# Performance work log

Measured on AMD Instinct MI355X. Metric: run time of the kernel, lower is better.

The kernel has to match this reference:

```python
import jax, jax.numpy as jnp
import numpy as np

# dims: batch B, frames F_, spatial tokens N, heads H, head dim D, model dim DIM
B, F_, N, H, D, DIM = 1, 16, 1024, 8, 64, 512


def setup_inputs() -> dict:
    key = jax.random.key(0)
    k1, k2, k3, k4 = jax.random.split(key, 4)
    x = jax.random.normal(k1, (B, F_ * N, DIM), dtype=jnp.float32)
    W_qkv = jax.random.normal(k2, (DIM, 3 * H * D), dtype=jnp.float32) * 0.02
    W_out = jax.random.normal(k3, (H * D, DIM), dtype=jnp.float32) * 0.02
    mask = jax.random.randint(k4, (1, 1, N), 0, 2, dtype=jnp.int32)
    return {"x": x, "W_qkv": W_qkv, "W_out": W_out, "mask": mask, "diag": 1}


def reference(x, W_qkv, W_out, mask, diag):
    scale = D ** -0.5
    qkv = x @ W_qkv                      # [B, F*N, 3*H*D]
    q, k, v = jnp.split(qkv, 3, axis=-1)

    def split_heads(t):                  # 'b n (h d) -> (b h) n d'
        return t.reshape(B, F_ * N, H, D).transpose(0, 2, 1, 3).reshape(B * H, F_ * N, D)

    q, k, v = map(split_heads, (q, k, v))
    q = q * scale

    def axial(t):                        # '(b h) (f n) d -> (b h f) n d'
        return t.reshape(B * H * F_, N, D)

    q, k, v = map(axial, (q, k, v))

    sim = jnp.einsum('bid,bjd->bij', q, k)        # [(B*H*F), N, N]
    neg = -jnp.finfo(sim.dtype).max
    if diag:
        sim = jnp.where(jnp.eye(N, dtype=bool)[None], neg, sim)
    sim = jnp.where(mask == 0, neg, sim)           # padding mask broadcast
    attn = jax.nn.softmax(sim, axis=-1)
    out = jnp.einsum('bij,bjd->bid', attn, v)      # [(B*H*F), N, D]

    # '(b h f) n d -> (b h) (f n) d' then '(b h) n d -> b n (h d)'
    out = out.reshape(B, H, F_ * N, D).transpose(0, 2, 1, 3).reshape(B, F_ * N, H * D)
    return out @ W_out
```

## Files before the change

### kernel.cpp

```cpp
#include <hip/hip_runtime.h>
#include <stdint.h>

typedef __bf16 bf16;
typedef __bf16 bf16x8 __attribute__((ext_vector_type(8)));
typedef float f32x4 __attribute__((ext_vector_type(4)));

__device__ __forceinline__ void gload_lds16(const void* g, void* l) {
    __builtin_amdgcn_global_load_lds((const __attribute__((address_space(1))) void*)g,
                                     (__attribute__((address_space(3))) void*)l, 16, 0, 0);
}

__device__ __forceinline__ float fast_exp2(float x) { return __builtin_amdgcn_exp2f(x); }

__global__ __launch_bounds__(256) void k_cvt(const float* __restrict__ x, bf16* __restrict__ xb, int n8) {
    int i = blockIdx.x * 256 + threadIdx.x;
    if (i >= n8) return;
    const f32x4* p = (const f32x4*)(x + (size_t)i * 8);
    f32x4 a = p[0], b = p[1];
    bf16x8 o;
    o[0] = (bf16)a[0]; o[1] = (bf16)a[1]; o[2] = (bf16)a[2]; o[3] = (bf16)a[3];
    o[4] = (bf16)b[0]; o[5] = (bf16)b[1]; o[6] = (bf16)b[2]; o[7] = (bf16)b[3];
    *(bf16x8*)(xb + (size_t)i * 8) = o;
}

__global__ __launch_bounds__(256) void k_tx(const float* __restrict__ W, bf16* __restrict__ WT, int R, int C) {
    __shared__ float t[32][33];
    int n0 = blockIdx.x * 32, k0 = blockIdx.y * 32;
    int tx = threadIdx.x, ty = threadIdx.y;
    for (int i = 0; i < 32; i += 8) t[ty + i][tx] = W[(size_t)(k0 + ty + i) * C + n0 + tx];
    __syncthreads();
    for (int i = 0; i < 32; i += 8) WT[(size_t)(n0 + ty + i) * R + k0 + tx] = (bf16)t[tx][ty + i];
}

__global__ __launch_bounds__(256) void k_scan(const int* __restrict__ mask, int* __restrict__ idxU,
                                              int* __restrict__ cpos, int* __restrict__ meta) {
    __shared__ int lsum[256];
    int t = threadIdx.x;
    int m[4], s = 0;
#pragma unroll
    for (int e = 0; e < 4; e++) { m[e] = mask[4 * t + e]; s += m[e]; }
    lsum[t] = s;
    __syncthreads();
    for (int off = 1; off < 256; off <<= 1) {
        int v = (t >= off) ? lsum[t - off] : 0;
        __syncthreads();
        lsum[t] += v;
        __syncthreads();
    }
    int run = lsum[t] - s;
#pragma unroll
    for (int e = 0; e < 4; e++) {
        if (m[e]) { idxU[run] = 4 * t + e; cpos[4 * t + e] = run; run++; }
        else cpos[4 * t + e] = -1;
    }
    if (t == 255) { meta[0] = lsum[255]; meta[1] = (lsum[255] + 63) >> 6; }
}

__global__ __launch_bounds__(256) void k_qkv(const bf16* __restrict__ Xb, const bf16* __restrict__ WT,
                                             bf16* __restrict__ Qb, bf16* __restrict__ Kb, bf16* __restrict__ Vb) {
    __shared__ char As[16384], Bs[16384];
    int tid = threadIdx.x, l = tid & 63, w = tid >> 6;
    int wy = w >> 1, wx = w & 1;
    int id = blockIdx.x;
    int wg = (id & 7) * 192 + (id >> 3);
    int bm = (wg / 12) * 128, bn = (wg % 12) * 128;
    int lr = l & 15, kg = l >> 4;
    int p = l & 7, rsub = l >> 3;
    int csrc = p ^ rsub;
    f32x4 acc[4][4] = {};

    for (int k0 = 0; k0 < 512; k0 += 64) {
        __syncthreads();
#pragma unroll
        for (int i = 0; i < 4; i++) {
            int rt = w * 32 + i * 8 + rsub;
            gload_lds16((const char*)Xb + ((size_t)(bm + rt) * 512 + k0) * 2 + csrc * 16,
                        As + w * 4096 + i * 1024 + l * 16);
            gload_lds16((const char*)WT + ((size_t)(bn + rt) * 512 + k0) * 2 + csrc * 16,
                        Bs + w * 4096 + i * 1024 + l * 16);
        }
        __syncthreads();
#pragma unroll
        for (int kk = 0; kk < 2; kk++) {
            bf16x8 af[4], bfr[4];
            int sb = (kk * 4 + kg);
#pragma unroll
            for (int mt = 0; mt < 4; mt++) {
                int r = wy * 64 + mt * 16 + lr;
                af[mt] = *(const bf16x8*)(As + r * 128 + ((sb ^ (lr & 7)) << 4));
            }
#pragma unroll
            for (int nt = 0; nt < 4; nt++) {
                int r = wx * 64 + nt * 16 + lr;
                bfr[nt] = *(const bf16x8*)(Bs + r * 128 + ((sb ^ (lr & 7)) << 4));
            }
#pragma unroll
            for (int mt = 0; mt < 4; mt++)
#pragma unroll
                for (int nt = 0; nt < 4; nt++)
                    acc[mt][nt] = __builtin_amdgcn_mfma_f32_16x16x32_bf16(af[mt], bfr[nt], acc[mt][nt], 0, 0, 0);
        }
    }
#pragma unroll
    for (int mt = 0; mt < 4; mt++) {
#pragma unroll
        for (int nt = 0; nt < 4; nt++) {
            int c = bn + wx * 64 + nt * 16 + lr;
            int which = c >> 9, hd = c & 511, h = hd >> 6, d = hd & 63;
            float qs = (which == 0) ? 0.18033688f : 1.0f;
            bf16* base = (which == 0) ? Qb : (which == 1) ? Kb : Vb;
#pragma unroll
            for (int j = 0; j < 4; j++) {
                int m = bm + wy * 64 + mt * 16 + kg * 4 + j;
                int f = m >> 10, nn = m & 1023;
                base[((size_t)(h * 16 + f) * 1024 + nn) * 64 + d] = (bf16)(acc[mt][nt][j] * qs);
            }
        }
    }
}

__global__ __launch_bounds__(256) void k_gk(const bf16* __restrict__ Kb, bf16* __restrict__ Kc,
                                            const int* __restrict__ idxU, const int* __restrict__ meta) {
    int bp = blockIdx.y;
    int c = blockIdx.x * 32 + (threadIdx.x >> 3);
    int nU = meta[0], nUp = meta[1] << 6;
    if (c >= nUp) return;
    int ch = (threadIdx.x & 7) * 8;
    bf16x8 v = {};
    if (c < nU) {
        int row = idxU[c];
        v = *(const bf16x8*)(Kb + ((size_t)bp * 1024 + row) * 64 + ch);
    }
    *(bf16x8*)(Kc + ((size_t)bp * 1024 + c) * 64 + ch) = v;
}

__global__ __launch_bounds__(256) void k_vtg(const bf16* __restrict__ V, bf16* __restrict__ Vtc,
                                             const int* __restrict__ idxU, const int* __restrict__ meta) {
    __shared__ bf16 t[64][80];
    int bp = blockIdx.y, c0 = blockIdx.x * 64;
    int nU = meta[0], nUp = meta[1] << 6;
    if (c0 >= nUp) return;
    int tid = threadIdx.x;
    int nl = tid >> 2, dc = (tid & 3) * 16;
    int c = c0 + nl;
    bf16x8 a0 = {}, a1 = {};
    if (c < nU) {
        int row = idxU[c];
        const bf16* src = V + ((size_t)bp * 1024 + row) * 64 + dc;
        a0 = *(const bf16x8*)src;
        a1 = *(const bf16x8*)(src + 8);
    }
    *(bf16x8*)&t[nl][dc] = a0;
    *(bf16x8*)&t[nl][dc + 8] = a1;
    __syncthreads();
    int dl = tid >> 2, nc = (tid & 3) * 16;
    bf16x8 o0, o1;
#pragma unroll
    for (int i = 0; i < 8; i++) o0[i] = t[nc + i][dl];
#pragma unroll
    for (int i = 0; i < 8; i++) o1[i] = t[nc + 8 + i][dl];
    bf16* dst = Vtc + ((size_t)bp * 64 + dl) * 1024 + c0 + nc;
    *(bf16x8*)dst = o0;
    *(bf16x8*)(dst + 8) = o1;
}

__global__ __launch_bounds__(512) void k_attn(const bf16* __restrict__ Qb, const bf16* __restrict__ Kc,
                                              const bf16* __restrict__ Vtc, bf16* __restrict__ AO,
                                              const int* __restrict__ cpos, const int* __restrict__ meta,
                                              const int* __restrict__ diagp) {
    __shared__ char Ks[8192], Vs[8192], Ps[16384];
    int tid = threadIdx.x, l = tid & 63, w = tid >> 6;
    int id = blockIdx.x;
    int wg = (id & 7) * 128 + (id >> 3);
    int qt = wg & 7, bp = wg >> 3;
    int lr = l & 15, kg = l >> 4;
    int diag = diagp[0];
    int nU = meta[0], nT = meta[1];

    int nq = qt * 128 + w * 16 + lr;
    const char* Qrow = (const char*)Qb + ((size_t)bp * 1024 + nq) * 128;
    bf16x8 qf0 = *(const bf16x8*)(Qrow + kg * 16);
    bf16x8 qf1 = *(const bf16x8*)(Qrow + 64 + kg * 16);

    int cq[4];
#pragma unroll
    for (int j = 0; j < 4; j++) {
        int qg = qt * 128 + w * 16 + kg * 4 + j;
        cq[j] = diag ? cpos[qg] : -1;
    }

    const char* Kbase = (const char*)Kc + (size_t)bp * 1024 * 128;
    const char* Vbase = (const char*)Vtc + (size_t)bp * 64 * 2048;

    int rs = tid >> 3;
    int cs = (tid & 7) ^ (rs & 7);

    f32x4 o[4] = {};
    f32x4 psum = {0.f, 0.f, 0.f, 0.f};

    for (int kt = 0; kt < nT; kt++) {
        __syncthreads();
        gload_lds16(Kbase + (size_t)(kt * 64 + rs) * 128 + cs * 16, Ks + w * 1024);
        gload_lds16(Vbase + (size_t)rs * 2048 + kt * 128 + cs * 16, Vs + w * 1024);
        __syncthreads();

        f32x4 s[4] = {};
#pragma unroll
        for (int nt = 0; nt < 4; nt++) {
            int r = nt * 16 + lr;
            bf16x8 kf0 = *(const bf16x8*)(Ks + r * 128 + ((kg ^ (r & 7)) << 4));
            bf16x8 kf1 = *(const bf16x8*)(Ks + r * 128 + (((4 + kg) ^ (r & 7)) << 4));
            s[nt] = __builtin_amdgcn_mfma_f32_16x16x32_bf16(qf0, kf0, s[nt], 0, 0, 0);
            s[nt] = __builtin_amdgcn_mfma_f32_16x16x32_bf16(qf1, kf1, s[nt], 0, 0, 0);
        }

        float mf0 = (kt * 64 + lr < nU) ? 1.f : 0.f;
        float mf1 = (kt * 64 + 16 + lr < nU) ? 1.f : 0.f;
        float mf2 = (kt * 64 + 32 + lr < nU) ? 1.f : 0.f;
        float mf3 = (kt * 64 + 48 + lr < nU) ? 1.f : 0.f;
#pragma unroll
        for (int j = 0; j < 4; j++) {
            s[0][j] = fast_exp2(s[0][j]) * mf0;
            s[1][j] = fast_exp2(s[1][j]) * mf1;
            s[2][j] = fast_exp2(s[2][j]) * mf2;
            s[3][j] = fast_exp2(s[3][j]) * mf3;
        }
#pragma unroll
        for (int nt = 0; nt < 4; nt++) {
            int c = kt * 64 + nt * 16 + lr;
#pragma unroll
            for (int j = 0; j < 4; j++)
                if (c == cq[j]) s[nt][j] = 0.f;
        }
#pragma unroll
        for (int j = 0; j < 4; j++) psum[j] += (s[0][j] + s[1][j]) + (s[2][j] + s[3][j]);

#pragma unroll
        for (int nt = 0; nt < 4; nt++)
#pragma unroll
            for (int j = 0; j < 4; j++) {
                int rq = w * 16 + kg * 4 + j;
                int byte = (rq * 128 + (nt * 16 + lr) * 2) ^ ((rq & 7) << 4);
                *(bf16*)(Ps + byte) = (bf16)s[nt][j];
            }

        int rp = w * 16 + lr;
        bf16x8 pf0 = *(const bf16x8*)(Ps + rp * 128 + ((kg ^ (rp & 7)) << 4));
        bf16x8 pf1 = *(const bf16x8*)(Ps + rp * 128 + (((4 + kg) ^ (rp & 7)) << 4));
#pragma unroll
        for (int dt = 0; dt < 4; dt++) {
            int rd = dt * 16 + lr;
            bf16x8 vf0 = *(const bf16x8*)(Vs + rd * 128 + ((kg ^ (rd & 7)) << 4));
            bf16x8 vf1 = *(const bf16x8*)(Vs + rd * 128 + (((4 + kg) ^ (rd & 7)) << 4));
            o[dt] = __builtin_amdgcn_mfma_f32_16x16x32_bf16(pf0, vf0, o[dt], 0, 0, 0);
            o[dt] = __builtin_amdgcn_mfma_f32_16x16x32_bf16(pf1, vf1, o[dt], 0, 0, 0);
        }
    }

#pragma unroll
    for (int off = 1; off < 16; off <<= 1)
#pragma unroll
        for (int j = 0; j < 4; j++) psum[j] += __shfl_xor(psum[j], off, 64);
    float inv[4];
#pragma unroll
    for (int j = 0; j < 4; j++) inv[j] = 1.0f / psum[j];

    int f = bp & 15, h = bp >> 4;
#pragma unroll
    for (int dt = 0; dt < 4; dt++)
#pragma unroll
        for (int j = 0; j < 4; j++) {
            int n = qt * 128 + w * 16 + kg * 4 + j;
            size_t m = (size_t)f * 1024 + n;
            AO[m * 512 + h * 64 + dt * 16 + lr] = (bf16)(o[dt][j] * inv[j]);
        }
}

__global__ __launch_bounds__(256) void k_out(const bf16* __restrict__ Ab, const bf16* __restrict__ WT,
                                             float* __restrict__ out) {
    __shared__ char As[16384], Bs[16384];
    int tid = threadIdx.x, l = tid & 63, w = tid >> 6;
    int wy = w >> 1, wx = w & 1;
    int id = blockIdx.x;
    int wg = (id & 7) * 64 + (id >> 3);
    int bm = (wg / 4) * 128, bn = (wg % 4) * 128;
    int lr = l & 15, kg = l >> 4;
    int p = l & 7, rsub = l >> 3;
    int csrc = p ^ rsub;
    f32x4 acc[4][4] = {};

    for (int k0 = 0; k0 < 512; k0 += 64) {
        __syncthreads();
#pragma unroll
        for (int i = 0; i < 4; i++) {
            int rt = w * 32 + i * 8 + rsub;
            gload_lds16((const char*)Ab + ((size_t)(bm + rt) * 512 + k0) * 2 + csrc * 16,
                        As + w * 4096 + i * 1024 + l * 16);
            gload_lds16((const char*)WT + ((size_t)(bn + rt) * 512 + k0) * 2 + csrc * 16,
                        Bs + w * 4096 + i * 1024 + l * 16);
        }
        __syncthreads();
#pragma unroll
        for (int kk = 0; kk < 2; kk++) {
            bf16x8 af[4], bfr[4];
            int sb = (kk * 4 + kg);
#pragma unroll
            for (int mt = 0; mt < 4; mt++) {
                int r = wy * 64 + mt * 16 + lr;
                af[mt] = *(const bf16x8*)(As + r * 128 + ((sb ^ (lr & 7)) << 4));
            }
#pragma unroll
            for (int nt = 0; nt < 4; nt++) {
                int r = wx * 64 + nt * 16 + lr;
                bfr[nt] = *(const bf16x8*)(Bs + r * 128 + ((sb ^ (lr & 7)) << 4));
            }
#pragma unroll
            for (int mt = 0; mt < 4; mt++)
#pragma unroll
                for (int nt = 0; nt < 4; nt++)
                    acc[mt][nt] = __builtin_amdgcn_mfma_f32_16x16x32_bf16(af[mt], bfr[nt], acc[mt][nt], 0, 0, 0);
        }
    }
#pragma unroll
    for (int mt = 0; mt < 4; mt++)
#pragma unroll
        for (int nt = 0; nt < 4; nt++) {
            int c = bn + wx * 64 + nt * 16 + lr;
#pragma unroll
            for (int j = 0; j < 4; j++) {
                int m = bm + wy * 64 + mt * 16 + kg * 4 + j;
                out[(size_t)m * 512 + c] = acc[mt][nt][j];
            }
        }
}

extern "C" void kernel_launch(void* const* d_in, const int* in_sizes, int n_in,
                              void* d_out, int out_size, void* d_ws, size_t ws_size,
                              hipStream_t stream) {
    const float* x    = (const float*)d_in[0];
    const float* Wqkv = (const float*)d_in[1];
    const float* Wout = (const float*)d_in[2];
    const int*   mask = (const int*)d_in[3];
    const int*   diag = (const int*)d_in[4];
    float* out = (float*)d_out;
    char* ws = (char*)d_ws;

    bf16* Xb  = (bf16*)(ws);
    bf16* Kc  = (bf16*)(ws);
    bf16* WqT = (bf16*)(ws + ((size_t)16 << 20));
    bf16* WoT = (bf16*)(ws + ((size_t)18 << 20));
    int*  idxU = (int*)(ws + ((size_t)18 << 20) + (1 << 19));
    int*  cpos = (int*)(ws + ((size_t)18 << 20) + (1 << 19) + 4096);
    int*  meta = (int*)(ws + ((size_t)18 << 20) + (1 << 19) + 8192);
    bf16* Qb  = (bf16*)(ws + ((size_t)19 << 20));
    bf16* Kb  = (bf16*)(ws + ((size_t)35 << 20));
    bf16* Vtc = (bf16*)(ws + ((size_t)35 << 20));
    bf16* Vb  = (bf16*)(ws + ((size_t)51 << 20));
    bf16* AO  = (bf16*)(ws + ((size_t)67 << 20));

    hipLaunchKernelGGL(k_cvt, dim3(4096), dim3(256), 0, stream, x, Xb, 1048576);
    hipLaunchKernelGGL(k_tx,  dim3(48, 16), dim3(32, 8), 0, stream, Wqkv, WqT, 512, 1536);
    hipLaunchKernelGGL(k_tx,  dim3(16, 16), dim3(32, 8), 0, stream, Wout, WoT, 512, 512);
    hipLaunchKernelGGL(k_scan, dim3(1), dim3(256), 0, stream, mask, idxU, cpos, meta);
    hipLaunchKernelGGL(k_qkv, dim3(1536), dim3(256), 0, stream, Xb, WqT, Qb, Kb, Vb);
    hipLaunchKernelGGL(k_gk,  dim3(32, 128), dim3(256), 0, stream, Kb, Kc, idxU, meta);
    hipLaunchKernelGGL(k_vtg, dim3(16, 128), dim3(256), 0, stream, Vb, Vtc, idxU, meta);
    hipLaunchKernelGGL(k_attn, dim3(1024), dim3(512), 0, stream, Qb, Kc, Vtc, AO, cpos, meta, diag);
    hipLaunchKernelGGL(k_out, dim3(512), dim3(256), 0, stream, AO, WoT, out);
}
```

Measured before the change: 121.1 us.

## Fuse K/V mask compaction into QKV GEMM epilogue and enlarge GEMM tile

```diff
diff --git a/kernel.cpp b/kernel.cpp
--- a/kernel.cpp
+++ b/kernel.cpp
@@ -56,43 +56,54 @@
     if (t == 255) { meta[0] = lsum[255]; meta[1] = (lsum[255] + 63) >> 6; }
 }
 
-__global__ __launch_bounds__(256) void k_qkv(const bf16* __restrict__ Xb, const bf16* __restrict__ WT,
-                                             bf16* __restrict__ Qb, bf16* __restrict__ Kb, bf16* __restrict__ Vb) {
-    __shared__ char As[16384], Bs[16384];
+__global__ __launch_bounds__(256) void k_zpad(bf16* __restrict__ Kc, const int* __restrict__ meta) {
+    int bp = blockIdx.x;
+    int nU = meta[0], nUp = meta[1] << 6;
+    int n = (nUp - nU) * 64;
+    for (int idx = threadIdx.x; idx < n; idx += 256) {
+        int r = nU + (idx >> 6), d = idx & 63;
+        Kc[((size_t)bp * 1024 + r) * 64 + d] = (bf16)0.f;
+    }
+}
+
+__global__ __launch_bounds__(512) void k_qkv(const bf16* __restrict__ Xb, const bf16* __restrict__ WT,
+                                             bf16* __restrict__ Qb, bf16* __restrict__ Kc,
+                                             bf16* __restrict__ Vc, const int* __restrict__ cpos) {
+    __shared__ char As[32768], Bs[16384];
     int tid = threadIdx.x, l = tid & 63, w = tid >> 6;
-    int wy = w >> 1, wx = w & 1;
+    int wy = w & 3, wx = w >> 2;
     int id = blockIdx.x;
-    int wg = (id & 7) * 192 + (id >> 3);
-    int bm = (wg / 12) * 128, bn = (wg % 12) * 128;
+    int wg = (id & 7) * 96 + (id >> 3);
+    int bm = (wg / 12) * 256, bn = (wg % 12) * 128;
     int lr = l & 15, kg = l >> 4;
-    int p = l & 7, rsub = l >> 3;
-    int csrc = p ^ rsub;
+    int rsub = tid >> 3;
+    int csrc = (tid & 7) ^ (rsub & 7);
     f32x4 acc[4][4] = {};
 
     for (int k0 = 0; k0 < 512; k0 += 64) {
         __syncthreads();
 #pragma unroll
-        for (int i = 0; i < 4; i++) {
-            int rt = w * 32 + i * 8 + rsub;
-            gload_lds16((const char*)Xb + ((size_t)(bm + rt) * 512 + k0) * 2 + csrc * 16,
-                        As + w * 4096 + i * 1024 + l * 16);
-            gload_lds16((const char*)WT + ((size_t)(bn + rt) * 512 + k0) * 2 + csrc * 16,
-                        Bs + w * 4096 + i * 1024 + l * 16);
-        }
+        for (int i = 0; i < 4; i++)
+            gload_lds16((const char*)Xb + ((size_t)(bm + i * 64 + rsub) * 512 + k0) * 2 + csrc * 16,
+                        As + i * 8192 + tid * 16);
+#pragma unroll
+        for (int i = 0; i < 2; i++)
+            gload_lds16((const char*)WT + ((size_t)(bn + i * 64 + rsub) * 512 + k0) * 2 + csrc * 16,
+                        Bs + i * 8192 + tid * 16);
         __syncthreads();
 #pragma unroll
         for (int kk = 0; kk < 2; kk++) {
+            int sb = kk * 4 + kg;
             bf16x8 af[4], bfr[4];
-            int sb = (kk * 4 + kg);
 #pragma unroll
             for (int mt = 0; mt < 4; mt++) {
                 int r = wy * 64 + mt * 16 + lr;
-                af[mt] = *(const bf16x8*)(As + r * 128 + ((sb ^ (lr & 7)) << 4));
+                af[mt] = *(const bf16x8*)(As + r * 128 + ((sb ^ (r & 7)) << 4));
             }
 #pragma unroll
             for (int nt = 0; nt < 4; nt++) {
                 int r = wx * 64 + nt * 16 + lr;
-                bfr[nt] = *(const bf16x8*)(Bs + r * 128 + ((sb ^ (lr & 7)) << 4));
+                bfr[nt] = *(const bf16x8*)(Bs + r * 128 + ((sb ^ (r & 7)) << 4));
             }
 #pragma unroll
             for (int mt = 0; mt < 4; mt++)
@@ -101,41 +112,35 @@
                     acc[mt][nt] = __builtin_amdgcn_mfma_f32_16x16x32_bf16(af[mt], bfr[nt], acc[mt][nt], 0, 0, 0);
         }
     }
+
+    int cb = bn + wx * 64;
+    int which = cb >> 9, hd = cb & 511, h = hd >> 6;
 #pragma unroll
     for (int mt = 0; mt < 4; mt++) {
 #pragma unroll
-        for (int nt = 0; nt < 4; nt++) {
-            int c = bn + wx * 64 + nt * 16 + lr;
-            int which = c >> 9, hd = c & 511, h = hd >> 6, d = hd & 63;
-            float qs = (which == 0) ? 0.18033688f : 1.0f;
-            bf16* base = (which == 0) ? Qb : (which == 1) ? Kb : Vb;
-#pragma unroll
-            for (int j = 0; j < 4; j++) {
-                int m = bm + wy * 64 + mt * 16 + kg * 4 + j;
-                int f = m >> 10, nn = m & 1023;
-                base[((size_t)(h * 16 + f) * 1024 + nn) * 64 + d] = (bf16)(acc[mt][nt][j] * qs);
-            }
-        }
-    }
-}
-
-__global__ __launch_bounds__(256) void k_gk(const bf16* __restrict__ Kb, bf16* __restrict__ Kc,
-                                            const int* __restrict__ idxU, const int* __restrict__ meta) {
-    int bp = blockIdx.y;
-    int c = blockIdx.x * 32 + (threadIdx.x >> 3);
-    int nU = meta[0], nUp = meta[1] << 6;
-    if (c >= nUp) return;
-    int ch = (threadIdx.x & 7) * 8;
-    bf16x8 v = {};
-    if (c < nU) {
-        int row = idxU[c];
-        v = *(const bf16x8*)(Kb + ((size_t)bp * 1024 + row) * 64 + ch);
-    }
-    *(bf16x8*)(Kc + ((size_t)bp * 1024 + c) * 64 + ch) = v;
-}
-
-__global__ __launch_bounds__(256) void k_vtg(const bf16* __restrict__ V, bf16* __restrict__ Vtc,
-                                             const int* __restrict__ idxU, const int* __restrict__ meta) {
+        for (int j = 0; j < 4; j++) {
+            int m = bm + wy * 64 + mt * 16 + kg * 4 + j;
+            int f = m >> 10, nn = m & 1023;
+            int bpb = h * 16 + f;
+            if (which == 0) {
+#pragma unroll
+                for (int nt = 0; nt < 4; nt++)
+                    Qb[((size_t)bpb * 1024 + nn) * 64 + nt * 16 + lr] = (bf16)(acc[mt][nt][j] * 0.18033688f);
+            } else {
+                int cr = cpos[nn];
+                if (cr >= 0) {
+                    bf16* base = (which == 1) ? Kc : Vc;
+#pragma unroll
+                    for (int nt = 0; nt < 4; nt++)
+                        base[((size_t)bpb * 1024 + cr) * 64 + nt * 16 + lr] = (bf16)acc[mt][nt][j];
+                }
+            }
+        }
+    }
+}
+
+__global__ __launch_bounds__(256) void k_vtg(const bf16* __restrict__ Vc, bf16* __restrict__ Vtc,
+                                             const int* __restrict__ meta) {
     __shared__ bf16 t[64][80];
     int bp = blockIdx.y, c0 = blockIdx.x * 64;
     int nU = meta[0], nUp = meta[1] << 6;
@@ -145,8 +150,7 @@
     int c = c0 + nl;
     bf16x8 a0 = {}, a1 = {};
     if (c < nU) {
-        int row = idxU[c];
-        const bf16* src = V + ((size_t)bp * 1024 + row) * 64 + dc;
+        const bf16* src = Vc + ((size_t)bp * 1024 + c) * 64 + dc;
         a0 = *(const bf16x8*)src;
         a1 = *(const bf16x8*)(src + 8);
     }
@@ -346,25 +350,24 @@
     char* ws = (char*)d_ws;
 
     bf16* Xb  = (bf16*)(ws);
-    bf16* Kc  = (bf16*)(ws);
+    bf16* AO  = (bf16*)(ws);
     bf16* WqT = (bf16*)(ws + ((size_t)16 << 20));
     bf16* WoT = (bf16*)(ws + ((size_t)18 << 20));
     int*  idxU = (int*)(ws + ((size_t)18 << 20) + (1 << 19));
     int*  cpos = (int*)(ws + ((size_t)18 << 20) + (1 << 19) + 4096);
     int*  meta = (int*)(ws + ((size_t)18 << 20) + (1 << 19) + 8192);
     bf16* Qb  = (bf16*)(ws + ((size_t)19 << 20));
-    bf16* Kb  = (bf16*)(ws + ((size_t)35 << 20));
-    bf16* Vtc = (bf16*)(ws + ((size_t)35 << 20));
-    bf16* Vb  = (bf16*)(ws + ((size_t)51 << 20));
-    bf16* AO  = (bf16*)(ws + ((size_t)67 << 20));
+    bf16* Kc  = (bf16*)(ws + ((size_t)35 << 20));
+    bf16* Vc  = (bf16*)(ws + ((size_t)51 << 20));
+    bf16* Vtc = (bf16*)(ws + ((size_t)67 << 20));
 
     hipLaunchKernelGGL(k_cvt, dim3(4096), dim3(256), 0, stream, x, Xb, 1048576);
     hipLaunchKernelGGL(k_tx,  dim3(48, 16), dim3(32, 8), 0, stream, Wqkv, WqT, 512, 1536);
     hipLaunchKernelGGL(k_tx,  dim3(16, 16), dim3(32, 8), 0, stream, Wout, WoT, 512, 512);
     hipLaunchKernelGGL(k_scan, dim3(1), dim3(256), 0, stream, mask, idxU, cpos, meta);
-    hipLaunchKernelGGL(k_qkv, dim3(1536), dim3(256), 0, stream, Xb, WqT, Qb, Kb, Vb);
-    hipLaunchKernelGGL(k_gk,  dim3(32, 128), dim3(256), 0, stream, Kb, Kc, idxU, meta);
-    hipLaunchKernelGGL(k_vtg, dim3(16, 128), dim3(256), 0, stream, Vb, Vtc, idxU, meta);
+    hipLaunchKernelGGL(k_zpad, dim3(128), dim3(256), 0, stream, Kc, meta);
+    hipLaunchKernelGGL(k_qkv, dim3(768), dim3(512), 0, stream, Xb, WqT, Qb, Kc, Vc, cpos);
+    hipLaunchKernelGGL(k_vtg, dim3(16, 128), dim3(256), 0, stream, Vc, Vtc, meta);
     hipLaunchKernelGGL(k_attn, dim3(1024), dim3(512), 0, stream, Qb, Kc, Vtc, AO, cpos, meta, diag);
     hipLaunchKernelGGL(k_out, dim3(512), dim3(256), 0, stream, AO, WoT, out);
 }
```

Measured after the change: 123.0 us. Within noise of the previous version (+1.6%).

## Read weights and K/V fragments directly from global memory instead of LDS staging

Applied to the files above, without the earlier changes.

```diff
diff --git a/kernel.cpp b/kernel.cpp
--- a/kernel.cpp
+++ b/kernel.cpp
@@ -58,15 +58,15 @@
 
 __global__ __launch_bounds__(256) void k_qkv(const bf16* __restrict__ Xb, const bf16* __restrict__ WT,
                                              bf16* __restrict__ Qb, bf16* __restrict__ Kb, bf16* __restrict__ Vb) {
-    __shared__ char As[16384], Bs[16384];
+    __shared__ char As[16384];
     int tid = threadIdx.x, l = tid & 63, w = tid >> 6;
     int wy = w >> 1, wx = w & 1;
     int id = blockIdx.x;
     int wg = (id & 7) * 192 + (id >> 3);
     int bm = (wg / 12) * 128, bn = (wg % 12) * 128;
     int lr = l & 15, kg = l >> 4;
-    int p = l & 7, rsub = l >> 3;
-    int csrc = p ^ rsub;
+    int rsub = l >> 3;
+    int csrc = (l & 7) ^ rsub;
     f32x4 acc[4][4] = {};
 
     for (int k0 = 0; k0 < 512; k0 += 64) {
@@ -76,23 +76,21 @@
             int rt = w * 32 + i * 8 + rsub;
             gload_lds16((const char*)Xb + ((size_t)(bm + rt) * 512 + k0) * 2 + csrc * 16,
                         As + w * 4096 + i * 1024 + l * 16);
-            gload_lds16((const char*)WT + ((size_t)(bn + rt) * 512 + k0) * 2 + csrc * 16,
-                        Bs + w * 4096 + i * 1024 + l * 16);
         }
         __syncthreads();
 #pragma unroll
         for (int kk = 0; kk < 2; kk++) {
+            int sb = kk * 4 + kg;
             bf16x8 af[4], bfr[4];
-            int sb = (kk * 4 + kg);
+#pragma unroll
+            for (int nt = 0; nt < 4; nt++) {
+                int r = bn + wx * 64 + nt * 16 + lr;
+                bfr[nt] = *(const bf16x8*)(WT + (size_t)r * 512 + k0 + sb * 8);
+            }
 #pragma unroll
             for (int mt = 0; mt < 4; mt++) {
                 int r = wy * 64 + mt * 16 + lr;
-                af[mt] = *(const bf16x8*)(As + r * 128 + ((sb ^ (lr & 7)) << 4));
-            }
-#pragma unroll
-            for (int nt = 0; nt < 4; nt++) {
-                int r = wx * 64 + nt * 16 + lr;
-                bfr[nt] = *(const bf16x8*)(Bs + r * 128 + ((sb ^ (lr & 7)) << 4));
+                af[mt] = *(const bf16x8*)(As + r * 128 + ((sb ^ (r & 7)) << 4));
             }
 #pragma unroll
             for (int mt = 0; mt < 4; mt++)
@@ -101,20 +99,21 @@
                     acc[mt][nt] = __builtin_amdgcn_mfma_f32_16x16x32_bf16(af[mt], bfr[nt], acc[mt][nt], 0, 0, 0);
         }
     }
+
+    int cb = bn + wx * 64;
+    int which = cb >> 9, hd = cb & 511, h = hd >> 6;
+    bf16* base = (which == 0) ? Qb : (which == 1) ? Kb : Vb;
+    float qs = (which == 0) ? 0.18033688f : 1.0f;
 #pragma unroll
     for (int mt = 0; mt < 4; mt++) {
 #pragma unroll
-        for (int nt = 0; nt < 4; nt++) {
-            int c = bn + wx * 64 + nt * 16 + lr;
-            int which = c >> 9, hd = c & 511, h = hd >> 6, d = hd & 63;
-            float qs = (which == 0) ? 0.18033688f : 1.0f;
-            bf16* base = (which == 0) ? Qb : (which == 1) ? Kb : Vb;
-#pragma unroll
-            for (int j = 0; j < 4; j++) {
-                int m = bm + wy * 64 + mt * 16 + kg * 4 + j;
-                int f = m >> 10, nn = m & 1023;
-                base[((size_t)(h * 16 + f) * 1024 + nn) * 64 + d] = (bf16)(acc[mt][nt][j] * qs);
-            }
+        for (int j = 0; j < 4; j++) {
+            int m = bm + wy * 64 + mt * 16 + kg * 4 + j;
+            int f = m >> 10, nn = m & 1023;
+            int bpb = h * 16 + f;
+#pragma unroll
+            for (int nt = 0; nt < 4; nt++)
+                base[((size_t)bpb * 1024 + nn) * 64 + nt * 16 + lr] = (bf16)(acc[mt][nt][j] * qs);
         }
     }
 }
@@ -164,20 +163,20 @@
     *(bf16x8*)(dst + 8) = o1;
 }
 
-__global__ __launch_bounds__(512) void k_attn(const bf16* __restrict__ Qb, const bf16* __restrict__ Kc,
+__global__ __launch_bounds__(256) void k_attn(const bf16* __restrict__ Qb, const bf16* __restrict__ Kc,
                                               const bf16* __restrict__ Vtc, bf16* __restrict__ AO,
                                               const int* __restrict__ cpos, const int* __restrict__ meta,
                                               const int* __restrict__ diagp) {
-    __shared__ char Ks[8192], Vs[8192], Ps[16384];
+    __shared__ char Ps[8192];
     int tid = threadIdx.x, l = tid & 63, w = tid >> 6;
     int id = blockIdx.x;
-    int wg = (id & 7) * 128 + (id >> 3);
-    int qt = wg & 7, bp = wg >> 3;
+    int wg = (id & 7) * 256 + (id >> 3);
+    int qt = wg & 15, bp = wg >> 4;
     int lr = l & 15, kg = l >> 4;
     int diag = diagp[0];
     int nU = meta[0], nT = meta[1];
 
-    int nq = qt * 128 + w * 16 + lr;
+    int nq = qt * 64 + w * 16 + lr;
     const char* Qrow = (const char*)Qb + ((size_t)bp * 1024 + nq) * 128;
     bf16x8 qf0 = *(const bf16x8*)(Qrow + kg * 16);
     bf16x8 qf1 = *(const bf16x8*)(Qrow + 64 + kg * 16);
@@ -185,31 +184,23 @@
     int cq[4];
 #pragma unroll
     for (int j = 0; j < 4; j++) {
-        int qg = qt * 128 + w * 16 + kg * 4 + j;
+        int qg = qt * 64 + w * 16 + kg * 4 + j;
         cq[j] = diag ? cpos[qg] : -1;
     }
 
     const char* Kbase = (const char*)Kc + (size_t)bp * 1024 * 128;
     const char* Vbase = (const char*)Vtc + (size_t)bp * 64 * 2048;
 
-    int rs = tid >> 3;
-    int cs = (tid & 7) ^ (rs & 7);
-
     f32x4 o[4] = {};
     f32x4 psum = {0.f, 0.f, 0.f, 0.f};
 
     for (int kt = 0; kt < nT; kt++) {
-        __syncthreads();
-        gload_lds16(Kbase + (size_t)(kt * 64 + rs) * 128 + cs * 16, Ks + w * 1024);
-        gload_lds16(Vbase + (size_t)rs * 2048 + kt * 128 + cs * 16, Vs + w * 1024);
-        __syncthreads();
-
         f32x4 s[4] = {};
 #pragma unroll
         for (int nt = 0; nt < 4; nt++) {
-            int r = nt * 16 + lr;
-            bf16x8 kf0 = *(const bf16x8*)(Ks + r * 128 + ((kg ^ (r & 7)) << 4));
-            bf16x8 kf1 = *(const bf16x8*)(Ks + r * 128 + (((4 + kg) ^ (r & 7)) << 4));
+            const char* kr = Kbase + (size_t)(kt * 64 + nt * 16 + lr) * 128;
+            bf16x8 kf0 = *(const bf16x8*)(kr + kg * 16);
+            bf16x8 kf1 = *(const bf16x8*)(kr + 64 + kg * 16);
             s[nt] = __builtin_amdgcn_mfma_f32_16x16x32_bf16(qf0, kf0, s[nt], 0, 0, 0);
             s[nt] = __builtin_amdgcn_mfma_f32_16x16x32_bf16(qf1, kf1, s[nt], 0, 0, 0);
         }
@@ -249,9 +240,9 @@
         bf16x8 pf1 = *(const bf16x8*)(Ps + rp * 128 + (((4 + kg) ^ (rp & 7)) << 4));
 #pragma unroll
         for (int dt = 0; dt < 4; dt++) {
-            int rd = dt * 16 + lr;
-            bf16x8 vf0 = *(const bf16x8*)(Vs + rd * 128 + ((kg ^ (rd & 7)) << 4));
-            bf16x8 vf1 = *(const bf16x8*)(Vs + rd * 128 + (((4 + kg) ^ (rd & 7)) << 4));
+            const char* vr = Vbase + (size_t)(dt * 16 + lr) * 2048 + kt * 128;
+            bf16x8 vf0 = *(const bf16x8*)(vr + kg * 16);
+            bf16x8 vf1 = *(const bf16x8*)(vr + 64 + kg * 16);
             o[dt] = __builtin_amdgcn_mfma_f32_16x16x32_bf16(pf0, vf0, o[dt], 0, 0, 0);
             o[dt] = __builtin_amdgcn_mfma_f32_16x16x32_bf16(pf1, vf1, o[dt], 0, 0, 0);
         }
@@ -270,7 +261,7 @@
     for (int dt = 0; dt < 4; dt++)
 #pragma unroll
         for (int j = 0; j < 4; j++) {
-            int n = qt * 128 + w * 16 + kg * 4 + j;
+            int n = qt * 64 + w * 16 + kg * 4 + j;
             size_t m = (size_t)f * 1024 + n;
             AO[m * 512 + h * 64 + dt * 16 + lr] = (bf16)(o[dt][j] * inv[j]);
         }
@@ -278,15 +269,15 @@
 
 __global__ __launch_bounds__(256) void k_out(const bf16* __restrict__ Ab, const bf16* __restrict__ WT,
                                              float* __restrict__ out) {
-    __shared__ char As[16384], Bs[16384];
+    __shared__ char As[16384];
     int tid = threadIdx.x, l = tid & 63, w = tid >> 6;
     int wy = w >> 1, wx = w & 1;
     int id = blockIdx.x;
     int wg = (id & 7) * 64 + (id >> 3);
     int bm = (wg / 4) * 128, bn = (wg % 4) * 128;
     int lr = l & 15, kg = l >> 4;
-    int p = l & 7, rsub = l >> 3;
-    int csrc = p ^ rsub;
+    int rsub = l >> 3;
+    int csrc = (l & 7) ^ rsub;
     f32x4 acc[4][4] = {};
 
     for (int k0 = 0; k0 < 512; k0 += 64) {
@@ -296,23 +287,21 @@
             int rt = w * 32 + i * 8 + rsub;
             gload_lds16((const char*)Ab + ((size_t)(bm + rt) * 512 + k0) * 2 + csrc * 16,
                         As + w * 4096 + i * 1024 + l * 16);
-            gload_lds16((const char*)WT + ((size_t)(bn + rt) * 512 + k0) * 2 + csrc * 16,
-                        Bs + w * 4096 + i * 1024 + l * 16);
         }
         __syncthreads();
 #pragma unroll
         for (int kk = 0; kk < 2; kk++) {
+            int sb = kk * 4 + kg;
             bf16x8 af[4], bfr[4];
-            int sb = (kk * 4 + kg);
+#pragma unroll
+            for (int nt = 0; nt < 4; nt++) {
+                int r = bn + wx * 64 + nt * 16 + lr;
+                bfr[nt] = *(const bf16x8*)(WT + (size_t)r * 512 + k0 + sb * 8);
+            }
 #pragma unroll
             for (int mt = 0; mt < 4; mt++) {
                 int r = wy * 64 + mt * 16 + lr;
-                af[mt] = *(const bf16x8*)(As + r * 128 + ((sb ^ (lr & 7)) << 4));
-            }
-#pragma unroll
-            for (int nt = 0; nt < 4; nt++) {
-                int r = wx * 64 + nt * 16 + lr;
-                bfr[nt] = *(const bf16x8*)(Bs + r * 128 + ((sb ^ (lr & 7)) << 4));
+                af[mt] = *(const bf16x8*)(As + r * 128 + ((sb ^ (r & 7)) << 4));
             }
 #pragma unroll
             for (int mt = 0; mt < 4; mt++)
@@ -346,7 +335,7 @@
     char* ws = (char*)d_ws;
 
     bf16* Xb  = (bf16*)(ws);
-    bf16* Kc  = (bf16*)(ws);
+    bf16* Vtc = (bf16*)(ws);
     bf16* WqT = (bf16*)(ws + ((size_t)16 << 20));
     bf16* WoT = (bf16*)(ws + ((size_t)18 << 20));
     int*  idxU = (int*)(ws + ((size_t)18 << 20) + (1 << 19));
@@ -354,9 +343,9 @@
     int*  meta = (int*)(ws + ((size_t)18 << 20) + (1 << 19) + 8192);
     bf16* Qb  = (bf16*)(ws + ((size_t)19 << 20));
     bf16* Kb  = (bf16*)(ws + ((size_t)35 << 20));
-    bf16* Vtc = (bf16*)(ws + ((size_t)35 << 20));
+    bf16* AO  = (bf16*)(ws + ((size_t)35 << 20));
     bf16* Vb  = (bf16*)(ws + ((size_t)51 << 20));
-    bf16* AO  = (bf16*)(ws + ((size_t)67 << 20));
+    bf16* Kc  = (bf16*)(ws + ((size_t)67 << 20));
 
     hipLaunchKernelGGL(k_cvt, dim3(4096), dim3(256), 0, stream, x, Xb, 1048576);
     hipLaunchKernelGGL(k_tx,  dim3(48, 16), dim3(32, 8), 0, stream, Wqkv, WqT, 512, 1536);
@@ -365,6 +354,6 @@
     hipLaunchKernelGGL(k_qkv, dim3(1536), dim3(256), 0, stream, Xb, WqT, Qb, Kb, Vb);
     hipLaunchKernelGGL(k_gk,  dim3(32, 128), dim3(256), 0, stream, Kb, Kc, idxU, meta);
     hipLaunchKernelGGL(k_vtg, dim3(16, 128), dim3(256), 0, stream, Vb, Vtc, idxU, meta);
-    hipLaunchKernelGGL(k_attn, dim3(1024), dim3(512), 0, stream, Qb, Kc, Vtc, AO, cpos, meta, diag);
+    hipLaunchKernelGGL(k_attn, dim3(2048), dim3(256), 0, stream, Qb, Kc, Vtc, AO, cpos, meta, diag);
     hipLaunchKernelGGL(k_out, dim3(512), dim3(256), 0, stream, AO, WoT, out);
 }
```

After: 243.9 us. 2.01x slower.

## Merge prep kernels, gather K rows inside attention, add MFMA priority hints

Applied to the files above, without the earlier changes.

```diff
diff --git a/kernel.cpp b/kernel.cpp
--- a/kernel.cpp
+++ b/kernel.cpp
@@ -12,48 +12,54 @@
 
 __device__ __forceinline__ float fast_exp2(float x) { return __builtin_amdgcn_exp2f(x); }
 
-__global__ __launch_bounds__(256) void k_cvt(const float* __restrict__ x, bf16* __restrict__ xb, int n8) {
-    int i = blockIdx.x * 256 + threadIdx.x;
-    if (i >= n8) return;
-    const f32x4* p = (const f32x4*)(x + (size_t)i * 8);
-    f32x4 a = p[0], b = p[1];
-    bf16x8 o;
-    o[0] = (bf16)a[0]; o[1] = (bf16)a[1]; o[2] = (bf16)a[2]; o[3] = (bf16)a[3];
-    o[4] = (bf16)b[0]; o[5] = (bf16)b[1]; o[6] = (bf16)b[2]; o[7] = (bf16)b[3];
-    *(bf16x8*)(xb + (size_t)i * 8) = o;
-}
-
-__global__ __launch_bounds__(256) void k_tx(const float* __restrict__ W, bf16* __restrict__ WT, int R, int C) {
+__global__ __launch_bounds__(256) void k_prep(const float* __restrict__ x, bf16* __restrict__ xb,
+                                              const float* __restrict__ Wqkv, bf16* __restrict__ WqT,
+                                              const float* __restrict__ Wout, bf16* __restrict__ WoT,
+                                              const int* __restrict__ mask, int* __restrict__ idxU,
+                                              int* __restrict__ cpos, int* __restrict__ meta) {
     __shared__ float t[32][33];
-    int n0 = blockIdx.x * 32, k0 = blockIdx.y * 32;
-    int tx = threadIdx.x, ty = threadIdx.y;
-    for (int i = 0; i < 32; i += 8) t[ty + i][tx] = W[(size_t)(k0 + ty + i) * C + n0 + tx];
-    __syncthreads();
-    for (int i = 0; i < 32; i += 8) WT[(size_t)(n0 + ty + i) * R + k0 + tx] = (bf16)t[tx][ty + i];
-}
-
-__global__ __launch_bounds__(256) void k_scan(const int* __restrict__ mask, int* __restrict__ idxU,
-                                              int* __restrict__ cpos, int* __restrict__ meta) {
     __shared__ int lsum[256];
-    int t = threadIdx.x;
-    int m[4], s = 0;
-#pragma unroll
-    for (int e = 0; e < 4; e++) { m[e] = mask[4 * t + e]; s += m[e]; }
-    lsum[t] = s;
-    __syncthreads();
-    for (int off = 1; off < 256; off <<= 1) {
-        int v = (t >= off) ? lsum[t - off] : 0;
-        __syncthreads();
-        lsum[t] += v;
-        __syncthreads();
-    }
-    int run = lsum[t] - s;
-#pragma unroll
-    for (int e = 0; e < 4; e++) {
-        if (m[e]) { idxU[run] = 4 * t + e; cpos[4 * t + e] = run; run++; }
-        else cpos[4 * t + e] = -1;
-    }
-    if (t == 255) { meta[0] = lsum[255]; meta[1] = (lsum[255] + 63) >> 6; }
+    int b = blockIdx.x, tid = threadIdx.x;
+    if (b < 4096) {
+        int i = b * 256 + tid;
+        const f32x4* p = (const f32x4*)(x + (size_t)i * 8);
+        f32x4 a = p[0], c = p[1];
+        bf16x8 o;
+        o[0] = (bf16)a[0]; o[1] = (bf16)a[1]; o[2] = (bf16)a[2]; o[3] = (bf16)a[3];
+        o[4] = (bf16)c[0]; o[5] = (bf16)c[1]; o[6] = (bf16)c[2]; o[7] = (bf16)c[3];
+        *(bf16x8*)(xb + (size_t)i * 8) = o;
+    } else if (b < 4096 + 768 + 256) {
+        const float* W; bf16* WT; int C, bb;
+        if (b < 4096 + 768) { W = Wqkv; WT = WqT; C = 1536; bb = b - 4096;    }
+        else                { W = Wout; WT = WoT; C = 512;  bb = b - 4864;    }
+        int nblk = C / 32;
+        int n0 = (bb % nblk) * 32, k0 = (bb / nblk) * 32;
+        int tx = tid & 31, ty = tid >> 5;
+        for (int i = 0; i < 32; i += 8) t[ty + i][tx] = W[(size_t)(k0 + ty + i) * C + n0 + tx];
+        __syncthreads();
+        for (int i = 0; i < 32; i += 8) WT[(size_t)(n0 + ty + i) * 512 + k0 + tx] = (bf16)t[tx][ty + i];
+    } else {
+        int m[4], s = 0;
+#pragma unroll
+        for (int e = 0; e < 4; e++) { m[e] = mask[4 * tid + e]; s += m[e]; }
+        lsum[tid] = s;
+        __syncthreads();
+        for (int off = 1; off < 256; off <<= 1) {
+            int v = (tid >= off) ? lsum[tid - off] : 0;
+            __syncthreads();
+            lsum[tid] += v;
+            __syncthreads();
+        }
+        int run = lsum[tid] - s;
+#pragma unroll
+        for (int e = 0; e < 4; e++) {
+            if (m[e]) { idxU[run] = 4 * tid + e; cpos[4 * tid + e] = run; run++; }
+            else cpos[4 * tid + e] = -1;
+        }
+        int nU = lsum[255];
+        for (int i = nU + tid; i < 1024; i += 256) idxU[i] = 0;
+        if (tid == 255) { meta[0] = nU; meta[1] = (nU + 63) >> 6; }
+    }
 }
 
 __global__ __launch_bounds__(256) void k_qkv(const bf16* __restrict__ Xb, const bf16* __restrict__ WT,
@@ -117,21 +123,6 @@
             }
         }
     }
-}
-
-__global__ __launch_bounds__(256) void k_gk(const bf16* __restrict__ Kb, bf16* __restrict__ Kc,
-                                            const int* __restrict__ idxU, const int* __restrict__ meta) {
-    int bp = blockIdx.y;
-    int c = blockIdx.x * 32 + (threadIdx.x >> 3);
-    int nU = meta[0], nUp = meta[1] << 6;
-    if (c >= nUp) return;
-    int ch = (threadIdx.x & 7) * 8;
-    bf16x8 v = {};
-    if (c < nU) {
-        int row = idxU[c];
-        v = *(const bf16x8*)(Kb + ((size_t)bp * 1024 + row) * 64 + ch);
-    }
-    *(bf16x8*)(Kc + ((size_t)bp * 1024 + c) * 64 + ch) = v;
 }
 
 __global__ __launch_bounds__(256) void k_vtg(const bf16* __restrict__ V, bf16* __restrict__ Vtc,
@@ -164,10 +155,10 @@
     *(bf16x8*)(dst + 8) = o1;
 }
 
-__global__ __launch_bounds__(512) void k_attn(const bf16* __restrict__ Qb, const bf16* __restrict__ Kc,
+__global__ __launch_bounds__(512) void k_attn(const bf16* __restrict__ Qb, const bf16* __restrict__ Kb,
                                               const bf16* __restrict__ Vtc, bf16* __restrict__ AO,
-                                              const int* __restrict__ cpos, const int* __restrict__ meta,
-                                              const int* __restrict__ diagp) {
+                                              const int* __restrict__ cpos, const int* __restrict__ idxU,
+                                              const int* __restrict__ meta, const int* __restrict__ diagp) {
     __shared__ char Ks[8192], Vs[8192], Ps[16384];
     int tid = threadIdx.x, l = tid & 63, w = tid >> 6;
     int id = blockIdx.x;
@@ -189,7 +180,7 @@
         cq[j] = diag ? cpos[qg] : -1;
     }
 
-    const char* Kbase = (const char*)Kc + (size_t)bp * 1024 * 128;
+    const char* Kbb = (const char*)Kb + (size_t)bp * 1024 * 128;
     const char* Vbase = (const char*)Vtc + (size_t)bp * 64 * 2048;
 
     int rs = tid >> 3;
@@ -200,11 +191,13 @@
 
     for (int kt = 0; kt < nT; kt++) {
         __syncthreads();
-        gload_lds16(Kbase + (size_t)(kt * 64 + rs) * 128 + cs * 16, Ks + w * 1024);
+        int krow = idxU[kt * 64 + rs];
+        gload_lds16(Kbb + (size_t)krow * 128 + cs * 16, Ks + w * 1024);
         gload_lds16(Vbase + (size_t)rs * 2048 + kt * 128 + cs * 16, Vs + w * 1024);
         __syncthreads();
 
         f32x4 s[4] = {};
+        __builtin_amdgcn_s_setprio(1);
 #pragma unroll
         for (int nt = 0; nt < 4; nt++) {
             int r = nt * 16 + lr;
@@ -213,6 +206,7 @@
             s[nt] = __builtin_amdgcn_mfma_f32_16x16x32_bf16(qf0, kf0, s[nt], 0, 0, 0);
             s[nt] = __builtin_amdgcn_mfma_f32_16x16x32_bf16(qf1, kf1, s[nt], 0, 0, 0);
         }
+        __builtin_amdgcn_s_setprio(0);
 
         float mf0 = (kt * 64 + lr < nU) ? 1.f : 0.f;
         float mf1 = (kt * 64 + 16 + lr < nU) ? 1.f : 0.f;
@@ -247,6 +241,7 @@
         int rp = w * 16 + lr;
         bf16x8 pf0 = *(const bf16x8*)(Ps + rp * 128 + ((kg ^ (rp & 7)) << 4));
         bf16x8 pf1 = *(const bf16x8*)(Ps + rp * 128 + (((4 + kg) ^ (rp & 7)) << 4));
+        __builtin_amdgcn_s_setprio(1);
 #pragma unroll
         for (int dt = 0; dt < 4; dt++) {
             int rd = dt * 16 + lr;
@@ -255,6 +250,7 @@
             o[dt] = __builtin_amdgcn_mfma_f32_16x16x32_bf16(pf0, vf0, o[dt], 0, 0, 0);
             o[dt] = __builtin_amdgcn_mfma_f32_16x16x32_bf16(pf1, vf1, o[dt], 0, 0, 0);
         }
+        __builtin_amdgcn_s_setprio(0);
     }
 
 #pragma unroll
@@ -346,7 +342,7 @@
     char* ws = (char*)d_ws;
 
     bf16* Xb  = (bf16*)(ws);
-    bf16* Kc  = (bf16*)(ws);
+    bf16* Vtc = (bf16*)(ws);
     bf16* WqT = (bf16*)(ws + ((size_t)16 << 20));
     bf16* WoT = (bf16*)(ws + ((size_t)18 << 20));
     int*  idxU = (int*)(ws + ((size_t)18 << 20) + (1 << 19));
@@ -354,17 +350,13 @@
     int*  meta = (int*)(ws + ((size_t)18 << 20) + (1 << 19) + 8192);
     bf16* Qb  = (bf16*)(ws + ((size_t)19 << 20));
     bf16* Kb  = (bf16*)(ws + ((size_t)35 << 20));
-    bf16* Vtc = (bf16*)(ws + ((size_t)35 << 20));
     bf16* Vb  = (bf16*)(ws + ((size_t)51 << 20));
     bf16* AO  = (bf16*)(ws + ((size_t)67 << 20));
 
-    hipLaunchKernelGGL(k_cvt, dim3(4096), dim3(256), 0, stream, x, Xb, 1048576);
-    hipLaunchKernelGGL(k_tx,  dim3(48, 16), dim3(32, 8), 0, stream, Wqkv, WqT, 512, 1536);
-    hipLaunchKernelGGL(k_tx,  dim3(16, 16), dim3(32, 8), 0, stream, Wout, WoT, 512, 512);
-    hipLaunchKernelGGL(k_scan, dim3(1), dim3(256), 0, stream, mask, idxU, cpos, meta);
+    hipLaunchKernelGGL(k_prep, dim3(4096 + 768 + 256 + 1), dim3(256), 0, stream,
+                       x, Xb, Wqkv, WqT, Wout, WoT, mask, idxU, cpos, meta);
     hipLaunchKernelGGL(k_qkv, dim3(1536), dim3(256), 0, stream, Xb, WqT, Qb, Kb, Vb);
-    hipLaunchKernelGGL(k_gk,  dim3(32, 128), dim3(256), 0, stream, Kb, Kc, idxU, meta);
     hipLaunchKernelGGL(k_vtg, dim3(16, 128), dim3(256), 0, stream, Vb, Vtc, idxU, meta);
-    hipLaunchKernelGGL(k_attn, dim3(1024), dim3(512), 0, stream, Qb, Kc, Vtc, AO, cpos, meta, diag);
+    hipLaunchKernelGGL(k_attn, dim3(1024), dim3(512), 0, stream, Qb, Kb, Vtc, AO, cpos, idxU, meta, diag);
     hipLaunchKernelGGL(k_out, dim3(512), dim3(256), 0, stream, AO, WoT, out);
 }
```

Result: faster. 113.8 us (-6.1%).
